# Kernel tuning notes

Measured on AMD Instinct MI355X. Metric: run time of the kernel, lower is better.

Reference implementation:

```python
import jax, jax.numpy as jnp
import numpy as np
import math, functools

QUERY_DIM = 64
HEADS = 4
DIM_HEAD = 16
INNER_DIM = HEADS * DIM_HEAD  # 64


def setup_inputs() -> dict:
    key = jax.random.key(0)
    k0, k1, k2, k3, k4, k5 = jax.random.split(key, 6)
    B, N, H = 4, 4096, 8
    s = 1.0 / math.sqrt(QUERY_DIM)
    return {
        "x": jax.random.normal(k0, (B, N, H, QUERY_DIM), dtype=jnp.float32),
        "Wq": jax.random.normal(k1, (QUERY_DIM, INNER_DIM), dtype=jnp.float32) * s,
        "Wk": jax.random.normal(k2, (QUERY_DIM, INNER_DIM), dtype=jnp.float32) * s,
        "Wv": jax.random.normal(k3, (QUERY_DIM, INNER_DIM), dtype=jnp.float32) * s,
        "Wo": jax.random.normal(k4, (INNER_DIM, QUERY_DIM), dtype=jnp.float32) * s,
        "bo": jnp.zeros((QUERY_DIM,), dtype=jnp.float32),
    }


def _query_chunk_size(n: int) -> int:
    # mirrors the module's chunk-size selection on flatten_latent_dim = shape[-3]
    if n % 64 == 0:
        return n // 64
    if n % 16 == 0:
        return n // 16
    if n % 4 == 0:
        return n // 4
    return n


def _chunked_attention(q, k, v, q_chunk):
    # q,k,v: (..., seq, h, d). Online-softmax chunking over queries; key_chunk_size
    # (16384) exceeds num_kv so a single key chunk is used -> per-q-chunk softmax
    # over the full key axis, which is exactly the same math as the original
    # max-rescaled accumulation.
    prec = jax.lax.Precision.HIGHEST
    scale = 1.0 / math.sqrt(k.shape[-1])
    q = q * scale
    nq = q.shape[-3]

    @functools.partial(jax.checkpoint, prevent_cse=False)
    def one_chunk(i):
        qc = jax.lax.dynamic_slice_in_dim(q, i, q_chunk, axis=-3)  # (..., qc, h, d)
        s = jnp.einsum('...qhd,...khd->...qhk', qc, k, precision=prec)
        a = jax.nn.softmax(s, axis=-1)  # stable: single max-subtract
        return jnp.einsum('...khf,...qhk->...qhf', v, a, precision=prec)

    res = jax.lax.map(one_chunk, jnp.arange(0, nq, q_chunk))  # (nchunks, ..., qc, h, f)
    return jnp.concatenate(res, axis=-3)  # (..., nq, h, f)


def reference(x, Wq, Wk, Wv, Wo, bo):
    # context = x (self-attention path)
    q = jnp.einsum('...d,df->...f', x, Wq)
    k = jnp.einsum('...d,df->...f', x, Wk)
    v = jnp.einsum('...d,df->...f', x, Wv)
    qcs = _query_chunk_size(q.shape[-3])
    hidden = _chunked_attention(q, k, v, qcs)
    return jnp.einsum('...f,fd->...d', hidden, Wo) + bo
```

## Files before the change

### kernel.cpp

```cpp
#include <hip/hip_runtime.h>
#include <hip/hip_bf16.h>

typedef __attribute__((ext_vector_type(8))) short short8;
typedef __attribute__((ext_vector_type(4))) float f32x4;
typedef __attribute__((ext_vector_type(8))) unsigned short ushort8;
typedef __attribute__((ext_vector_type(2))) unsigned uint2v;

#define LOG2E 1.44269504088896340736f

__device__ __forceinline__ float fexp2(float x) {
#if __has_builtin(__builtin_amdgcn_exp2f)
  return __builtin_amdgcn_exp2f(x);
#else
  return exp2f(x);
#endif
}
__device__ __forceinline__ unsigned cvtpk(float lo, float hi) {
  unsigned r;
  asm("v_cvt_pk_bf16_f32 %0, %1, %2" : "=v"(r) : "v"(lo), "v"(hi));
  return r;
}
__device__ __forceinline__ void pswap32(unsigned &a, unsigned &b) {
#if __has_builtin(__builtin_amdgcn_permlane32_swap)
  uint2v r = __builtin_amdgcn_permlane32_swap(a, b, false, false);
  a = r[0]; b = r[1];
#else
  asm("v_permlane32_swap_b32 %0, %1" : "+v"(a), "+v"(b));
#endif
}
__device__ __forceinline__ void pswap16(unsigned &a, unsigned &b) {
#if __has_builtin(__builtin_amdgcn_permlane16_swap)
  uint2v r = __builtin_amdgcn_permlane16_swap(a, b, false, false);
  a = r[0]; b = r[1];
#else
  asm("v_permlane16_swap_b32 %0, %1" : "+v"(a), "+v"(b));
#endif
}
__device__ __forceinline__ float redsum16(float x) {
  unsigned a = __float_as_uint(x), b = a;
  pswap16(a, b);
  return __uint_as_float(a) + __uint_as_float(b);
}
__device__ __forceinline__ float redsum32(float x) {
  unsigned a = __float_as_uint(x), b = a;
  pswap32(a, b);
  return __uint_as_float(a) + __uint_as_float(b);
}
__device__ __forceinline__ void gload_lds16(const unsigned short* g, unsigned short* l) {
  __builtin_amdgcn_global_load_lds(
      (const __attribute__((address_space(1))) unsigned int*)g,
      (__attribute__((address_space(3))) unsigned int*)l, 16, 0, 0);
}
__device__ __forceinline__ int swzK(int r) {
  return ((r & 3) | (((r >> 3) & 1) << 2)) << 3;
}

__global__ __launch_bounds__(256) void proj_kernel(
    const float* __restrict__ x,
    const float* __restrict__ Wq, const float* __restrict__ Wk,
    const float* __restrict__ Wv,
    unsigned short* __restrict__ Qo, unsigned short* __restrict__ Ko,
    unsigned short* __restrict__ Vto)
{
  const int tid = threadIdx.x, lane = tid & 63, w = tid >> 6;
  const int r15 = lane & 15, G = lane >> 4;
  const int bh = blockIdx.x >> 4, nt = blockIdx.x & 15;
  const int b = bh >> 3, h = bh & 7;
  const int n0 = nt * 256 + w * 64;

  short8 xf[4][2];
  #pragma unroll
  for (int ct = 0; ct < 4; ++ct) {
    const int n = n0 + ct * 16 + r15;
    const float* xr = x + ((size_t)((b * 4096 + n) * 8 + h)) * 64;
    #pragma unroll
    for (int s = 0; s < 2; ++s) {
      const f32x4 f0 = *(const f32x4*)&xr[s * 32 + G * 8];
      const f32x4 f1 = *(const f32x4*)&xr[s * 32 + G * 8 + 4];
      union { unsigned u[4]; short8 s8; } uu;
      uu.u[0] = cvtpk(f0[0], f0[1]); uu.u[1] = cvtpk(f0[2], f0[3]);
      uu.u[2] = cvtpk(f1[0], f1[1]); uu.u[3] = cvtpk(f1[2], f1[3]);
      xf[ct][s] = uu.s8;
    }
  }

  const size_t obase = (size_t)bh * (4096 * 64);

  #pragma unroll
  for (int wi = 0; wi < 2; ++wi) {
    const float* W = wi ? Wk : Wq;
    unsigned short* O = wi ? Ko : Qo;
    const float sc = wi ? 1.0f : 0.125f * LOG2E;
    short8 wf[4][2];
    #pragma unroll
    for (int ft = 0; ft < 4; ++ft)
      #pragma unroll
      for (int s = 0; s < 2; ++s) {
        union { unsigned u[4]; short8 s8; } uu;
        #pragma unroll
        for (int jj = 0; jj < 4; ++jj) {
          const int k0 = s * 32 + G * 8 + jj * 2;
          uu.u[jj] = cvtpk(W[k0 * 64 + ft * 16 + r15] * sc,
                           W[(k0 + 1) * 64 + ft * 16 + r15] * sc);
        }
        wf[ft][s] = uu.s8;
      }
    f32x4 acc[4][4];
    #pragma unroll
    for (int ft = 0; ft < 4; ++ft)
      #pragma unroll
      for (int ct = 0; ct < 4; ++ct) acc[ft][ct] = (f32x4){0.f, 0.f, 0.f, 0.f};
    #pragma unroll
    for (int s = 0; s < 2; ++s)
      #pragma unroll
      for (int ft = 0; ft < 4; ++ft)
        #pragma unroll
        for (int ct = 0; ct < 4; ++ct)
          acc[ft][ct] = __builtin_amdgcn_mfma_f32_16x16x32_bf16(
              wf[ft][s], xf[ct][s], acc[ft][ct], 0, 0, 0);
    #pragma unroll
    for (int ft = 0; ft < 4; ++ft)
      #pragma unroll
      for (int ct = 0; ct < 4; ++ct) {
        uint2v pk;
        pk[0] = cvtpk(acc[ft][ct][0], acc[ft][ct][1]);
        pk[1] = cvtpk(acc[ft][ct][2], acc[ft][ct][3]);
        *(uint2v*)&O[obase + (size_t)(n0 + ct * 16 + r15) * 64 + ft * 16 + G * 4] = pk;
      }
  }

  {
    short8 wf[4][2];
    #pragma unroll
    for (int ft = 0; ft < 4; ++ft)
      #pragma unroll
      for (int s = 0; s < 2; ++s) {
        union { unsigned u[4]; short8 s8; } uu;
        #pragma unroll
        for (int jj = 0; jj < 4; ++jj) {
          const int k0 = s * 32 + G * 8 + jj * 2;
          uu.u[jj] = cvtpk(Wv[k0 * 64 + ft * 16 + r15], Wv[(k0 + 1) * 64 + ft * 16 + r15]);
        }
        wf[ft][s] = uu.s8;
      }
    f32x4 acc[4][4];
    #pragma unroll
    for (int ct = 0; ct < 4; ++ct)
      #pragma unroll
      for (int ft = 0; ft < 4; ++ft) acc[ct][ft] = (f32x4){0.f, 0.f, 0.f, 0.f};
    #pragma unroll
    for (int s = 0; s < 2; ++s)
      #pragma unroll
      for (int ct = 0; ct < 4; ++ct)
        #pragma unroll
        for (int ft = 0; ft < 4; ++ft)
          acc[ct][ft] = __builtin_amdgcn_mfma_f32_16x16x32_bf16(
              xf[ct][s], wf[ft][s], acc[ct][ft], 0, 0, 0);
    #pragma unroll
    for (int ct = 0; ct < 4; ++ct)
      #pragma unroll
      for (int ft = 0; ft < 4; ++ft) {
        uint2v pk;
        pk[0] = cvtpk(acc[ct][ft][0], acc[ct][ft][1]);
        pk[1] = cvtpk(acc[ct][ft][2], acc[ct][ft][3]);
        *(uint2v*)&Vto[obase + (size_t)(ft * 16 + r15) * 4096 + n0 + ct * 16 + G * 4] = pk;
      }
  }
}

__global__ __launch_bounds__(256, 2) void attn_kernel(
    const unsigned short* __restrict__ Q, const unsigned short* __restrict__ K,
    const unsigned short* __restrict__ Vt, const float* __restrict__ Wo,
    const float* __restrict__ bo, float* __restrict__ out)
{
  __shared__ __align__(16) unsigned short SM[16384];

  const int tid = threadIdx.x;
  const int lane = tid & 63, w = tid >> 6;
  const int r15 = lane & 15, G = lane >> 4;

  int bid = blockIdx.x;
  bid = (bid & 7) * 64 + (bid >> 3);
  const int bh = bid >> 4, qt256 = bid & 15;

  const unsigned short* Qb = Q + (size_t)bh * (4096 * 64);
  const unsigned short* Kb = K + (size_t)bh * (4096 * 64);
  const unsigned short* Vb = Vt + (size_t)bh * (64 * 4096);
  const int q0w = qt256 * 256 + w * 64;

  short8 qf[4][2];
  #pragma unroll
  for (int qt = 0; qt < 4; ++qt) {
    const unsigned short* qr = Qb + (size_t)(q0w + qt * 16 + r15) * 64;
    qf[qt][0] = *(const short8*)&qr[G * 8];
    qf[qt][1] = *(const short8*)&qr[32 + G * 8];
  }

  f32x4 oacc[4][4];
  #pragma unroll
  for (int qt = 0; qt < 4; ++qt)
    #pragma unroll
    for (int t = 0; t < 4; ++t) oacc[qt][t] = (f32x4){0.f, 0.f, 0.f, 0.f};
  float lsum[4] = {0.f, 0.f, 0.f, 0.f};

  int kro[4][2], vro[4][2];
  {
    const int Rr = r15 >> 2, gg = r15 & 3;
    #pragma unroll
    for (int t = 0; t < 4; ++t) {
      const int row = gg + ((t & 1) << 2) + ((Rr & 1) << 3) + ((t >> 1) << 4) + ((Rr >> 1) << 5);
      const int sw = swzK(row);
      kro[t][0] = row * 64 + ((G * 8) ^ sw);
      kro[t][1] = row * 64 + ((32 + G * 8) ^ sw);
      const int vrow = t * 16 + r15;
      const int vs = (vrow & 7) << 3;
      vro[t][0] = vrow * 64 + ((G * 8) ^ vs);
      vro[t][1] = vrow * 64 + ((32 + G * 8) ^ vs);
    }
  }

  const int seg = w * 2;
  const int kr0 = seg * 8 + (lane >> 3), kr1 = kr0 + 8;
  const int c8 = (lane & 7) * 8;
  const int koff0 = kr0 * 64 + (c8 ^ swzK(kr0));
  const int koff1 = kr1 * 64 + (c8 ^ swzK(kr1));
  const int voff0 = kr0 * 4096 + (c8 ^ ((kr0 & 7) << 3));
  const int voff1 = kr1 * 4096 + (c8 ^ ((kr1 & 7) << 3));

  gload_lds16(Kb + koff0, &SM[seg * 512]);
  gload_lds16(Kb + koff1, &SM[(seg + 1) * 512]);
  gload_lds16(Vb + voff0, &SM[8192 + seg * 512]);
  gload_lds16(Vb + voff1, &SM[8192 + (seg + 1) * 512]);
  __syncthreads();

  int buf = 0;
  for (int kt = 0; kt < 64; ++kt) {
    if (kt < 63) {
      const int ko = (kt + 1) * 4096;
      const int vo = (kt + 1) * 64;
      unsigned short* kd = &SM[(buf ^ 1) * 4096];
      unsigned short* vd = &SM[8192 + (buf ^ 1) * 4096];
      gload_lds16(Kb + ko + koff0, kd + seg * 512);
      gload_lds16(Kb + ko + koff1, kd + (seg + 1) * 512);
      gload_lds16(Vb + vo + voff0, vd + seg * 512);
      gload_lds16(Vb + vo + voff1, vd + (seg + 1) * 512);
    }

    const unsigned short* Kc = &SM[buf * 4096];
    const unsigned short* Vc = &SM[8192 + buf * 4096];

    f32x4 s[4][4];
    #pragma unroll
    for (int t = 0; t < 4; ++t) {
      const short8 kf0 = *(const short8*)&Kc[kro[t][0]];
      const short8 kf1 = *(const short8*)&Kc[kro[t][1]];
      __builtin_amdgcn_s_setprio(1);
      #pragma unroll
      for (int qt = 0; qt < 4; ++qt) {
        f32x4 z = (f32x4){0.f, 0.f, 0.f, 0.f};
        z = __builtin_amdgcn_mfma_f32_16x16x32_bf16(kf0, qf[qt][0], z, 0, 0, 0);
        s[qt][t] = __builtin_amdgcn_mfma_f32_16x16x32_bf16(kf1, qf[qt][1], z, 0, 0, 0);
      }
      __builtin_amdgcn_s_setprio(0);
    }

    short8 pa[4][2];
    #pragma unroll
    for (int qt = 0; qt < 4; ++qt) {
      float p[4][4];
      #pragma unroll
      for (int t = 0; t < 4; ++t)
        #pragma unroll
        for (int g = 0; g < 4; ++g) p[t][g] = fexp2(s[qt][t][g]);
      const float r0 = (p[0][0] + p[0][1]) + (p[0][2] + p[0][3]);
      const float r1 = (p[1][0] + p[1][1]) + (p[1][2] + p[1][3]);
      const float r2 = (p[2][0] + p[2][1]) + (p[2][2] + p[2][3]);
      const float r3 = (p[3][0] + p[3][1]) + (p[3][2] + p[3][3]);
      lsum[qt] += (r0 + r1) + (r2 + r3);

      unsigned wA[4], wB[4];
      wA[0] = cvtpk(p[0][0], p[0][1]); wA[1] = cvtpk(p[0][2], p[0][3]);
      wA[2] = cvtpk(p[1][0], p[1][1]); wA[3] = cvtpk(p[1][2], p[1][3]);
      wB[0] = cvtpk(p[2][0], p[2][1]); wB[1] = cvtpk(p[2][2], p[2][3]);
      wB[2] = cvtpk(p[3][0], p[3][1]); wB[3] = cvtpk(p[3][2], p[3][3]);
      union { unsigned u[4]; short8 s8; } fa, fb;
      #pragma unroll
      for (int i = 0; i < 4; ++i) {
        pswap32(wA[i], wB[i]);
        fa.u[i] = wA[i];
        fb.u[i] = wB[i];
      }
      pa[qt][0] = fa.s8;
      pa[qt][1] = fb.s8;
    }

    #pragma unroll
    for (int t = 0; t < 4; ++t) {
      const short8 vb0 = *(const short8*)&Vc[vro[t][0]];
      const short8 vb1 = *(const short8*)&Vc[vro[t][1]];
      __builtin_amdgcn_s_setprio(1);
      #pragma unroll
      for (int qt = 0; qt < 4; ++qt) {
        oacc[qt][t] = __builtin_amdgcn_mfma_f32_16x16x32_bf16(pa[qt][0], vb0, oacc[qt][t], 0, 0, 0);
        oacc[qt][t] = __builtin_amdgcn_mfma_f32_16x16x32_bf16(pa[qt][1], vb1, oacc[qt][t], 0, 0, 0);
      }
      __builtin_amdgcn_s_setprio(0);
    }
    __syncthreads();
    buf ^= 1;
  }

  float lt[4];
  #pragma unroll
  for (int qt = 0; qt < 4; ++qt) {
    float l = lsum[qt];
    l = redsum16(l);
    l = redsum32(l);
    lt[qt] = l;
  }

  short8 wof[4][2];
  #pragma unroll
  for (int nt = 0; nt < 4; ++nt)
    #pragma unroll
    for (int st = 0; st < 2; ++st) {
      union { unsigned u[4]; short8 s8; } uu;
      #pragma unroll
      for (int jj = 0; jj < 4; ++jj) {
        const int k0 = st * 32 + G * 8 + jj * 2;
        uu.u[jj] = cvtpk(Wo[k0 * 64 + nt * 16 + r15], Wo[(k0 + 1) * 64 + nt * 16 + r15]);
      }
      wof[nt][st] = uu.s8;
    }
  float bov[4];
  #pragma unroll
  for (int nt = 0; nt < 4; ++nt) bov[nt] = bo[nt * 16 + r15];

  float* Ol = (float*)&SM[0] + w * 2048;
  const int b = bh >> 3, hh = bh & 7;

  #pragma unroll
  for (int pass = 0; pass < 2; ++pass) {
    #pragma unroll
    for (int ql = 0; ql < 2; ++ql) {
      const int qt = pass * 2 + ql;
      float li[4];
      #pragma unroll
      for (int g = 0; g < 4; ++g) li[g] = __builtin_amdgcn_rcpf(__shfl(lt[qt], G * 4 + g));
      #pragma unroll
      for (int t = 0; t < 4; ++t)
        #pragma unroll
        for (int g = 0; g < 4; ++g) {
          const int q = ql * 16 + G * 4 + g;
          const int d = t * 16 + r15;
          Ol[q * 64 + (d ^ ((q & 7) << 3))] = oacc[qt][t][g] * li[g];
        }
    }
    #pragma unroll
    for (int ql = 0; ql < 2; ++ql) {
      const int qt = pass * 2 + ql;
      short8 af[2];
      #pragma unroll
      for (int st = 0; st < 2; ++st) {
        const int row = ql * 16 + r15;
        const int c = (st * 32 + G * 8) ^ ((row & 7) << 3);
        const f32x4 f0 = *(const f32x4*)&Ol[row * 64 + c];
        const f32x4 f1 = *(const f32x4*)&Ol[row * 64 + c + 4];
        union { unsigned u[4]; short8 s8; } uu;
        uu.u[0] = cvtpk(f0[0], f0[1]); uu.u[1] = cvtpk(f0[2], f0[3]);
        uu.u[2] = cvtpk(f1[0], f1[1]); uu.u[3] = cvtpk(f1[2], f1[3]);
        af[st] = uu.s8;
      }
      #pragma unroll
      for (int nt = 0; nt < 4; ++nt) {
        f32x4 dacc = (f32x4){bov[nt], bov[nt], bov[nt], bov[nt]};
        dacc = __builtin_amdgcn_mfma_f32_16x16x32_bf16(af[0], wof[nt][0], dacc, 0, 0, 0);
        dacc = __builtin_amdgcn_mfma_f32_16x16x32_bf16(af[1], wof[nt][1], dacc, 0, 0, 0);
        #pragma unroll
        for (int g = 0; g < 4; ++g) {
          const int nq = q0w + qt * 16 + G * 4 + g;
          out[((size_t)(b * 4096 + nq) * 8 + hh) * 64 + nt * 16 + r15] = dacc[g];
        }
      }
    }
  }
}

extern "C" void kernel_launch(void* const* d_in, const int* in_sizes, int n_in,
                              void* d_out, int out_size, void* d_ws, size_t ws_size,
                              hipStream_t stream) {
  const float* x  = (const float*)d_in[0];
  const float* Wq = (const float*)d_in[1];
  const float* Wk = (const float*)d_in[2];
  const float* Wv = (const float*)d_in[3];
  const float* Wo = (const float*)d_in[4];
  const float* bo = (const float*)d_in[5];

  const size_t NE = 8388608;
  unsigned short* Qw  = (unsigned short*)d_ws;
  unsigned short* Kw  = Qw + NE;
  unsigned short* Vtw = Kw + NE;

  proj_kernel<<<512, 256, 0, stream>>>(x, Wq, Wk, Wv, Qw, Kw, Vtw);
  attn_kernel<<<512, 256, 0, stream>>>(Qw, Kw, Vtw, Wo, bo, (float*)d_out);
}
```

Measured before the change: 171.4 us.

## Halve attention block to two waves and double grid, drop setprio, inline exp asm

Shrinks each attention block from four waves covering 256 queries to two waves covering 128 queries, and launches 1024 blocks instead of 512. Each wave now issues four K and four V tile loads per step instead of two, so the cooperative loads are spread over fewer waves. It also removes the s_setprio hints around the MFMA groups and replaces the exp2 builtin with inline v_exp_f32 asm. The intent is better scheduling and occupancy across CUs. In exchange, K/V tiles are loaded from global memory twice as often overall, since each tile is now shared by half as many queries.

```diff
diff --git a/kernel.cpp b/kernel.cpp
--- a/kernel.cpp
+++ b/kernel.cpp
@@ -9,11 +9,9 @@
 #define LOG2E 1.44269504088896340736f
 
 __device__ __forceinline__ float fexp2(float x) {
-#if __has_builtin(__builtin_amdgcn_exp2f)
-  return __builtin_amdgcn_exp2f(x);
-#else
-  return exp2f(x);
-#endif
+  float r;
+  asm("v_exp_f32 %0, %1" : "=v"(r) : "v"(x));
+  return r;
 }
 __device__ __forceinline__ unsigned cvtpk(float lo, float hi) {
   unsigned r;
@@ -168,7 +166,7 @@
   }
 }
 
-__global__ __launch_bounds__(256, 2) void attn_kernel(
+__global__ __launch_bounds__(128) void attn_kernel(
     const unsigned short* __restrict__ Q, const unsigned short* __restrict__ K,
     const unsigned short* __restrict__ Vt, const float* __restrict__ Wo,
     const float* __restrict__ bo, float* __restrict__ out)
@@ -180,13 +178,13 @@
   const int r15 = lane & 15, G = lane >> 4;
 
   int bid = blockIdx.x;
-  bid = (bid & 7) * 64 + (bid >> 3);
-  const int bh = bid >> 4, qt256 = bid & 15;
+  bid = (bid & 7) * 128 + (bid >> 3);
+  const int bh = bid >> 5, qt128 = bid & 31;
 
   const unsigned short* Qb = Q + (size_t)bh * (4096 * 64);
   const unsigned short* Kb = K + (size_t)bh * (4096 * 64);
   const unsigned short* Vb = Vt + (size_t)bh * (64 * 4096);
-  const int q0w = qt256 * 256 + w * 64;
+  const int q0w = qt128 * 128 + w * 64;
 
   short8 qf[4][2];
   #pragma unroll
@@ -219,18 +217,23 @@
     }
   }
 
-  const int seg = w * 2;
-  const int kr0 = seg * 8 + (lane >> 3), kr1 = kr0 + 8;
+  const int segb = w * 4;
+  int koffs[4], voffs[4], ksegd[4], vsegd[4];
   const int c8 = (lane & 7) * 8;
-  const int koff0 = kr0 * 64 + (c8 ^ swzK(kr0));
-  const int koff1 = kr1 * 64 + (c8 ^ swzK(kr1));
-  const int voff0 = kr0 * 4096 + (c8 ^ ((kr0 & 7) << 3));
-  const int voff1 = kr1 * 4096 + (c8 ^ ((kr1 & 7) << 3));
-
-  gload_lds16(Kb + koff0, &SM[seg * 512]);
-  gload_lds16(Kb + koff1, &SM[(seg + 1) * 512]);
-  gload_lds16(Vb + voff0, &SM[8192 + seg * 512]);
-  gload_lds16(Vb + voff1, &SM[8192 + (seg + 1) * 512]);
+  #pragma unroll
+  for (int j = 0; j < 4; ++j) {
+    const int kr = (segb + j) * 8 + (lane >> 3);
+    koffs[j] = kr * 64 + (c8 ^ swzK(kr));
+    voffs[j] = kr * 4096 + (c8 ^ ((kr & 7) << 3));
+    ksegd[j] = (segb + j) * 512;
+    vsegd[j] = 8192 + (segb + j) * 512;
+  }
+
+  #pragma unroll
+  for (int j = 0; j < 4; ++j) {
+    gload_lds16(Kb + koffs[j], &SM[ksegd[j]]);
+    gload_lds16(Vb + voffs[j], &SM[vsegd[j]]);
+  }
   __syncthreads();
 
   int buf = 0;
@@ -238,12 +241,12 @@
     if (kt < 63) {
       const int ko = (kt + 1) * 4096;
       const int vo = (kt + 1) * 64;
-      unsigned short* kd = &SM[(buf ^ 1) * 4096];
-      unsigned short* vd = &SM[8192 + (buf ^ 1) * 4096];
-      gload_lds16(Kb + ko + koff0, kd + seg * 512);
-      gload_lds16(Kb + ko + koff1, kd + (seg + 1) * 512);
-      gload_lds16(Vb + vo + voff0, vd + seg * 512);
-      gload_lds16(Vb + vo + voff1, vd + (seg + 1) * 512);
+      const int bo2 = (buf ^ 1) * 4096;
+      #pragma unroll
+      for (int j = 0; j < 4; ++j) {
+        gload_lds16(Kb + ko + koffs[j], &SM[bo2 + ksegd[j]]);
+        gload_lds16(Vb + vo + voffs[j], &SM[bo2 + vsegd[j]]);
+      }
     }
 
     const unsigned short* Kc = &SM[buf * 4096];
@@ -254,14 +257,12 @@
     for (int t = 0; t < 4; ++t) {
       const short8 kf0 = *(const short8*)&Kc[kro[t][0]];
       const short8 kf1 = *(const short8*)&Kc[kro[t][1]];
-      __builtin_amdgcn_s_setprio(1);
       #pragma unroll
       for (int qt = 0; qt < 4; ++qt) {
         f32x4 z = (f32x4){0.f, 0.f, 0.f, 0.f};
         z = __builtin_amdgcn_mfma_f32_16x16x32_bf16(kf0, qf[qt][0], z, 0, 0, 0);
         s[qt][t] = __builtin_amdgcn_mfma_f32_16x16x32_bf16(kf1, qf[qt][1], z, 0, 0, 0);
       }
-      __builtin_amdgcn_s_setprio(0);
     }
 
     short8 pa[4][2];
@@ -298,13 +299,11 @@
     for (int t = 0; t < 4; ++t) {
       const short8 vb0 = *(const short8*)&Vc[vro[t][0]];
       const short8 vb1 = *(const short8*)&Vc[vro[t][1]];
-      __builtin_amdgcn_s_setprio(1);
       #pragma unroll
       for (int qt = 0; qt < 4; ++qt) {
         oacc[qt][t] = __builtin_amdgcn_mfma_f32_16x16x32_bf16(pa[qt][0], vb0, oacc[qt][t], 0, 0, 0);
         oacc[qt][t] = __builtin_amdgcn_mfma_f32_16x16x32_bf16(pa[qt][1], vb1, oacc[qt][t], 0, 0, 0);
       }
-      __builtin_amdgcn_s_setprio(0);
     }
     __syncthreads();
     buf ^= 1;
@@ -402,5 +401,5 @@
   unsigned short* Vtw = Kw + NE;
 
   proj_kernel<<<512, 256, 0, stream>>>(x, Wq, Wk, Wv, Qw, Kw, Vtw);
-  attn_kernel<<<512, 256, 0, stream>>>(Qw, Kw, Vtw, Wo, bo, (float*)d_out);
-}
+  attn_kernel<<<1024, 128, 0, stream>>>(Qw, Kw, Vtw, Wo, bo, (float*)d_out);
+}
```

Result: slower. 188.9 us (+10.2%).
